# Optimization experiments

Measured on AMD Instinct MI355X. Metric: run time of the kernel, lower is better.

## Reference

```python
import jax, jax.numpy as jnp
import numpy as np

EMBED_DIM = 768
N_HEADS = 12
HEAD_DIM = EMBED_DIM // N_HEADS
B, S = 8, 1024


def setup_inputs() -> dict:
    key = jax.random.key(0)
    ks = jax.random.split(key, 7)
    sc = 1.0 / np.sqrt(HEAD_DIM)
    return {
        "sequences": jax.random.normal(ks[0], (B, S, EMBED_DIM), dtype=jnp.float32),
        # per-head Linear weights stored [H, in, out] (torch Linear is x @ W.T + b;
        # with random init the layout convention is equivalent math)
        "Wq": jax.random.normal(ks[1], (N_HEADS, HEAD_DIM, HEAD_DIM), dtype=jnp.float32) * sc,
        "bq": jax.random.normal(ks[2], (N_HEADS, HEAD_DIM), dtype=jnp.float32) * 0.01,
        "Wk": jax.random.normal(ks[3], (N_HEADS, HEAD_DIM, HEAD_DIM), dtype=jnp.float32) * sc,
        "bk": jax.random.normal(ks[4], (N_HEADS, HEAD_DIM), dtype=jnp.float32) * 0.01,
        "Wv": jax.random.normal(ks[5], (N_HEADS, HEAD_DIM, HEAD_DIM), dtype=jnp.float32) * sc,
        "bv": jax.random.normal(ks[6], (N_HEADS, HEAD_DIM), dtype=jnp.float32) * 0.01,
    }


def reference(sequences, Wq, bq, Wk, bk, Wv, bv):
    b, s, d = sequences.shape
    h, hd = Wq.shape[0], Wq.shape[1]
    x = sequences.reshape(b, s, h, hd)              # split embed dim into heads
    q = jnp.einsum("bshd,hde->bshe", x, Wq) + bq    # per-head linear (block-diag GEMM)
    k = jnp.einsum("bshd,hde->bshe", x, Wk) + bk
    v = jnp.einsum("bshd,hde->bshe", x, Wv) + bv
    # NOTE: original module applies NO 1/sqrt(head_dim) scaling
    logits = jnp.einsum("bshe,bthe->bhst", q, k)    # [B,H,S,S]
    attn = jax.nn.softmax(logits, axis=-1)
    out = jnp.einsum("bhst,bthe->bshe", attn, v)    # [B,S,H,hd]
    return out.reshape(b, s, d)
```

## Files before the change

### kernel.cpp

```cpp
#include <hip/hip_runtime.h>
#include <stdint.h>

#define EMBED 768
#define NH 12
#define HD 64
#define Bsz 8
#define Ssz 1024
#define LOG2E 1.44269504088896f

typedef __attribute__((ext_vector_type(4))) float f32x4;
typedef __attribute__((ext_vector_type(16))) float f32x16;
typedef __attribute__((ext_vector_type(8))) _Float16 f16x8;
typedef __attribute__((ext_vector_type(4))) _Float16 f16x4;
typedef __attribute__((ext_vector_type(2))) _Float16 f16x2;
typedef __attribute__((ext_vector_type(2))) __fp16 h16x2;
typedef __attribute__((ext_vector_type(4))) unsigned int u32x4;
typedef __attribute__((ext_vector_type(2))) unsigned int u32x2;

__launch_bounds__(256)
__global__ void qkv_proj(const float* __restrict__ x,
                         const float* __restrict__ Wq, const float* __restrict__ bq,
                         const float* __restrict__ Wk, const float* __restrict__ bk,
                         const float* __restrict__ Wv, const float* __restrict__ bv,
                         _Float16* __restrict__ Qb, _Float16* __restrict__ Kb,
                         _Float16* __restrict__ Vt)
{
    __shared__ _Float16 XT[128 * 72];
    __shared__ _Float16 Wt[3 * 64 * 72];
    __shared__ float Bs[192];

    const int bt = blockIdx.x;
    const int st = bt & 7;
    const int h  = (bt >> 3) % NH;
    const int b  = bt / (8 * NH);
    const int sbase = st * 128;
    const int tid = threadIdx.x;
    const int lane = tid & 63, w = tid >> 6;
    const int l15 = lane & 15, quad = lane >> 4;

    for (int i = 0; i < 8; ++i) {
        int idx = tid + 256 * i;
        int row = idx >> 4;
        int c4  = (idx & 15) * 4;
        const float4 g = *(const float4*)&x[(size_t)(b * Ssz + sbase + row) * EMBED + h * HD + c4];
        f16x4 v; v[0] = (_Float16)g.x; v[1] = (_Float16)g.y; v[2] = (_Float16)g.z; v[3] = (_Float16)g.w;
        *(f16x4*)&XT[row * 72 + c4] = v;
    }
    {
        const float* Ws0[3] = {Wq, Wk, Wv};
        const float* bs0[3] = {bq, bk, bv};
#pragma unroll
        for (int m = 0; m < 3; ++m) {
            const float* W = Ws0[m] + (size_t)h * HD * HD;
            for (int i = 0; i < 4; ++i) {
                int idx = tid + 256 * i;
                int d = idx >> 4, e4 = (idx & 15) * 4;
                float4 g = *(const float4*)&W[d * 64 + e4];
                Wt[m * 4608 + (e4 + 0) * 72 + d] = (_Float16)g.x;
                Wt[m * 4608 + (e4 + 1) * 72 + d] = (_Float16)g.y;
                Wt[m * 4608 + (e4 + 2) * 72 + d] = (_Float16)g.z;
                Wt[m * 4608 + (e4 + 3) * 72 + d] = (_Float16)g.w;
            }
        }
        if (tid < 192) Bs[tid] = bs0[tid >> 6][h * HD + (tid & 63)];
    }
    __syncthreads();

    f16x8 bx[2][2];
    const int nbg0 = w * 2;
#pragma unroll
    for (int nb = 0; nb < 2; ++nb)
#pragma unroll
        for (int kh = 0; kh < 2; ++kh)
            bx[nb][kh] = *(const f16x8*)&XT[((nbg0 + nb) * 16 + l15) * 72 + kh * 32 + quad * 8];
    __syncthreads();

    const size_t qkbase = (size_t)(b * NH + h) * Ssz + sbase;
    const f32x4 zero = {0.f, 0.f, 0.f, 0.f};

#pragma unroll
    for (int m = 0; m < 3; ++m) {
        f32x4 acc[2][4];
#pragma unroll
        for (int nb = 0; nb < 2; ++nb)
#pragma unroll
            for (int eb = 0; eb < 4; ++eb) acc[nb][eb] = zero;
#pragma unroll
        for (int eb = 0; eb < 4; ++eb)
#pragma unroll
            for (int kh = 0; kh < 2; ++kh) {
                f16x8 aw = *(const f16x8*)&Wt[m * 4608 + (eb * 16 + l15) * 72 + kh * 32 + quad * 8];
#pragma unroll
                for (int nb = 0; nb < 2; ++nb)
                    acc[nb][eb] = __builtin_amdgcn_mfma_f32_16x16x32_f16(aw, bx[nb][kh], acc[nb][eb], 0, 0, 0);
            }

        if (m < 2) {
            const float sc = (m == 0) ? LOG2E : 1.0f;
#pragma unroll
            for (int nb = 0; nb < 2; ++nb)
#pragma unroll
                for (int eb = 0; eb < 4; ++eb) {
                    f32x4 bb = *(const f32x4*)&Bs[m * 64 + eb * 16 + quad * 4];
                    f16x4 v;
#pragma unroll
                    for (int r = 0; r < 4; ++r) v[r] = (_Float16)((acc[nb][eb][r] + bb[r]) * sc);
                    *(f16x4*)&XT[((nbg0 + nb) * 16 + l15) * 72 + eb * 16 + quad * 4] = v;
                }
            __syncthreads();
            _Float16* outp = (m == 0) ? Qb : Kb;
            for (int i = 0; i < 4; ++i) {
                int idx = tid + 256 * i;
                int s = idx >> 3, e8 = (idx & 7) * 8;
                *(f16x8*)&outp[(qkbase + s) * HD + e8] = *(const f16x8*)&XT[s * 72 + e8];
            }
            __syncthreads();
        } else {
            _Float16* Vs = XT;
#pragma unroll
            for (int nb = 0; nb < 2; ++nb)
#pragma unroll
                for (int eb = 0; eb < 4; ++eb) {
                    f32x4 bb = *(const f32x4*)&Bs[128 + eb * 16 + quad * 4];
#pragma unroll
                    for (int r = 0; r < 4; ++r)
                        Vs[(eb * 16 + quad * 4 + r) * 136 + (nbg0 + nb) * 16 + l15] =
                            (_Float16)(acc[nb][eb][r] + bb[r]);
                }
            __syncthreads();
            for (int i = 0; i < 4; ++i) {
                int idx = tid + 256 * i;
                int e = idx >> 4, s8 = (idx & 15) * 8;
                *(f16x8*)&Vt[((size_t)(b * NH + h) * 64 + e) * Ssz + sbase + s8] =
                    *(const f16x8*)&Vs[e * 136 + s8];
            }
        }
    }
}

#define KVB 8192
__launch_bounds__(256, 2)
__global__ void attn(const _Float16* __restrict__ Qb, const _Float16* __restrict__ Kb,
                     const _Float16* __restrict__ Vt, float* __restrict__ out)
{
    __shared__ _Float16 KV[3 * KVB];

    const int bt = blockIdx.x;
    const int hh = bt % 96;
    const int qt = bt / 96;
    const int h  = hh % NH;
    const int b  = hh / NH;

    const int tid  = threadIdx.x;
    const int lane = tid & 63, w = tid >> 6;
    const int l31  = lane & 31;
    const int hf   = lane >> 5;

    const size_t bh = (size_t)(b * NH + h);
    const _Float16* Qg = Qb + bh * Ssz * HD;
    const _Float16* Kg = Kb + bh * Ssz * HD;
    const _Float16* Vg = Vt + bh * (size_t)HD * Ssz;

    const int qrow = qt * 128 + w * 32 + l31;
    f16x8 aq[4];
#pragma unroll
    for (int kk = 0; kk < 4; ++kk)
        aq[kk] = *(const f16x8*)&Qg[(size_t)qrow * HD + kk * 16 + hf * 8];

    const int ca = tid, cb = tid + 256;
    const int ra = ca >> 3, ga = (ca & 7) ^ (ra & 7);
    const int rb = cb >> 3, gb = (cb & 7) ^ (rb & 7);
    const _Float16* Ka  = Kg + ra * HD + ga * 8;
    const _Float16* Kb2 = Kg + rb * HD + gb * 8;
    const _Float16* Va  = Vg + (size_t)ra * Ssz + ga * 8;
    const _Float16* Vb  = Vg + (size_t)rb * Ssz + gb * 8;

#define STAGE(buf, kt_) do {                                                            \
    __builtin_amdgcn_global_load_lds(                                                   \
        (const __attribute__((address_space(1))) void*)(Ka + (kt_) * 64 * HD),          \
        (__attribute__((address_space(3))) void*)&KV[(buf) * KVB + ca * 8], 16, 0, 0);  \
    __builtin_amdgcn_global_load_lds(                                                   \
        (const __attribute__((address_space(1))) void*)(Kb2 + (kt_) * 64 * HD),         \
        (__attribute__((address_space(3))) void*)&KV[(buf) * KVB + cb * 8], 16, 0, 0);  \
    __builtin_amdgcn_global_load_lds(                                                   \
        (const __attribute__((address_space(1))) void*)(Va + (kt_) * 64),               \
        (__attribute__((address_space(3))) void*)&KV[(buf) * KVB + 4096 + ca * 8], 16, 0, 0); \
    __builtin_amdgcn_global_load_lds(                                                   \
        (const __attribute__((address_space(1))) void*)(Vb + (kt_) * 64),               \
        (__attribute__((address_space(3))) void*)&KV[(buf) * KVB + 4096 + cb * 8], 16, 0, 0); \
} while (0)

    const int rsw = l31 * 64;
    const int sx  = (l31 & 7) << 3;
    const int ch  = hf * 8;

    STAGE(0, 0);
    STAGE(1, 1);

    f32x16 o0, o1, zero16;
#pragma unroll
    for (int i = 0; i < 16; ++i) { o0[i] = 0.f; o1[i] = 0.f; zero16[i] = 0.f; }
    float m_run = -INFINITY;
    float la = 0.f, lb = 0.f, lc = 0.f, ld = 0.f;
    h16x2 ones2; ones2[0] = (__fp16)1.0f; ones2[1] = (__fp16)1.0f;

    __asm__ __volatile__("s_waitcnt vmcnt(4)" ::: "memory");
    __syncthreads();

#pragma unroll
    for (int kt = 0; kt < 16; ++kt) {
        const int bc = kt % 3;
        const int bs = (kt + 2) % 3;

        if (kt < 14) STAGE(bs, kt + 2);

        const _Float16* Ksb = &KV[bc * KVB];
        const _Float16* Vsb = &KV[bc * KVB + 4096];

        f32x16 st0, st1;
        __builtin_amdgcn_s_setprio(1);
        {
            const int col0 = ch ^ sx;
            f16x8 ak0 = *(const f16x8*)&Ksb[rsw + col0];
            f16x8 ak1 = *(const f16x8*)&Ksb[2048 + rsw + col0];
            st0 = __builtin_amdgcn_mfma_f32_32x32x16_f16(ak0, aq[0], zero16, 0, 0, 0);
            st1 = __builtin_amdgcn_mfma_f32_32x32x16_f16(ak1, aq[0], zero16, 0, 0, 0);
        }
#pragma unroll
        for (int kk = 1; kk < 4; ++kk) {
            const int col = (kk * 16 + ch) ^ sx;
            f16x8 ak0 = *(const f16x8*)&Ksb[rsw + col];
            f16x8 ak1 = *(const f16x8*)&Ksb[2048 + rsw + col];
            st0 = __builtin_amdgcn_mfma_f32_32x32x16_f16(ak0, aq[kk], st0, 0, 0, 0);
            st1 = __builtin_amdgcn_mfma_f32_32x32x16_f16(ak1, aq[kk], st1, 0, 0, 0);
        }
        __builtin_amdgcn_s_setprio(0);

        float m8[8];
#pragma unroll
        for (int i = 0; i < 8; ++i)
            m8[i] = fmaxf(fmaxf(st0[i], st0[i + 8]), fmaxf(st1[i], st1[i + 8]));
        float m4a = fmaxf(m8[0], m8[4]), m4b = fmaxf(m8[1], m8[5]);
        float m4c = fmaxf(m8[2], m8[6]), m4d = fmaxf(m8[3], m8[7]);
        float mt = fmaxf(fmaxf(m4a, m4b), fmaxf(m4c, m4d));
        mt = fmaxf(mt, __shfl_xor(mt, 32, 64));

        if (__any(mt > m_run + 8.f)) {
            float mn = fmaxf(m_run, mt);
            float al = __builtin_amdgcn_exp2f(m_run - mn);
            m_run = mn;
            la *= al; lb *= al; lc *= al; ld *= al;
#pragma unroll
            for (int i = 0; i < 16; ++i) { o0[i] *= al; o1[i] *= al; }
        }

#pragma unroll
        for (int i = 0; i < 16; ++i) st0[i] = __builtin_amdgcn_exp2f(st0[i] - m_run);
#pragma unroll
        for (int i = 0; i < 16; ++i) st1[i] = __builtin_amdgcn_exp2f(st1[i] - m_run);

        __builtin_amdgcn_s_setprio(1);
#pragma unroll
        for (int kk = 0; kk < 4; ++kk) {
            const f32x16& pp = (kk < 2) ? st0 : st1;
            const int c = 8 * (kk & 1);
            h16x2 x0h = __builtin_amdgcn_cvt_pkrtz(pp[c+0], pp[c+1]);
            h16x2 x1h = __builtin_amdgcn_cvt_pkrtz(pp[c+2], pp[c+3]);
            h16x2 y0h = __builtin_amdgcn_cvt_pkrtz(pp[c+4], pp[c+5]);
            h16x2 y1h = __builtin_amdgcn_cvt_pkrtz(pp[c+6], pp[c+7]);
            la = __builtin_amdgcn_fdot2(x0h, ones2, la, false);
            lb = __builtin_amdgcn_fdot2(x1h, ones2, lb, false);
            lc = __builtin_amdgcn_fdot2(y0h, ones2, lc, false);
            ld = __builtin_amdgcn_fdot2(y1h, ones2, ld, false);
            unsigned X0 = __builtin_bit_cast(unsigned, x0h);
            unsigned X1 = __builtin_bit_cast(unsigned, x1h);
            unsigned Y0 = __builtin_bit_cast(unsigned, y0h);
            unsigned Y1 = __builtin_bit_cast(unsigned, y1h);
            u32x2 r02 = __builtin_amdgcn_permlane32_swap(X0, Y0, 0, 0);
            u32x2 r13 = __builtin_amdgcn_permlane32_swap(X1, Y1, 0, 0);
            u32x4 du = {r02[0], r13[0], r02[1], r13[1]};
            f16x8 bp = __builtin_bit_cast(f16x8, du);
            const int col = (kk * 16 + ch) ^ sx;
            f16x8 av0 = *(const f16x8*)&Vsb[rsw + col];
            f16x8 av1 = *(const f16x8*)&Vsb[2048 + rsw + col];
            o0 = __builtin_amdgcn_mfma_f32_32x32x16_f16(av0, bp, o0, 0, 0, 0);
            o1 = __builtin_amdgcn_mfma_f32_32x32x16_f16(av1, bp, o1, 0, 0, 0);
        }
        __builtin_amdgcn_s_setprio(0);

        if (kt < 14) {
            __asm__ __volatile__("s_waitcnt vmcnt(4)" ::: "memory");
            __syncthreads();
        } else if (kt < 15) {
            __asm__ __volatile__("s_waitcnt vmcnt(0)" ::: "memory");
            __syncthreads();
        }
    }

    float l_run = (la + lb) + (lc + ld);
    l_run += __shfl_xor(l_run, 32, 64);
    const float inv = 1.f / l_run;
    float* op = &out[((size_t)b * Ssz + qrow) * EMBED + h * HD];
#pragma unroll
    for (int r1 = 0; r1 < 4; ++r1) {
        f32x4 v0, v1;
#pragma unroll
        for (int r0 = 0; r0 < 4; ++r0) {
            v0[r0] = o0[4 * r1 + r0] * inv;
            v1[r0] = o1[4 * r1 + r0] * inv;
        }
        *(f32x4*)&op[r1 * 8 + hf * 4]      = v0;
        *(f32x4*)&op[32 + r1 * 8 + hf * 4] = v1;
    }
#undef STAGE
}

extern "C" void kernel_launch(void* const* d_in, const int* in_sizes, int n_in,
                              void* d_out, int out_size, void* d_ws, size_t ws_size,
                              hipStream_t stream) {
    const float* x  = (const float*)d_in[0];
    const float* Wq = (const float*)d_in[1];
    const float* bq = (const float*)d_in[2];
    const float* Wk = (const float*)d_in[3];
    const float* bk = (const float*)d_in[4];
    const float* Wv = (const float*)d_in[5];
    const float* bv = (const float*)d_in[6];

    _Float16* Qb = (_Float16*)d_ws;
    _Float16* Kb = Qb + (size_t)Bsz * NH * Ssz * HD;
    _Float16* Vt = Kb + (size_t)Bsz * NH * Ssz * HD;

    qkv_proj<<<dim3(Bsz * NH * 8), dim3(256), 0, stream>>>(x, Wq, bq, Wk, bk, Wv, bv, Qb, Kb, Vt);
    attn<<<dim3(Bsz * NH * 8), dim3(256), 0, stream>>>(Qb, Kb, Vt, (float*)d_out);
}
```

Baseline: 130.1 us.

## Fuse Q projection into attention kernel and switch KV staging to double buffer

The Q projection moves out of the projection kernel and into the attention kernel. Each attention block converts its own x tile and Wq to fp16 in LDS and computes Q with MFMA, so Q is no longer written to and re-read from the workspace. The K/V staging pipeline shrinks from triple to double buffering with a full vmcnt(0) wait every iteration, the kt loop is no longer unrolled, and the min-blocks-per-SM launch bound is dropped. This saves a Q round trip through global memory, but it adds per-block projection work in front of attention and exposes more load latency because less prefetch runs ahead.

After: 147.2 us. 13.1% more time.

```diff
diff --git a/kernel.cpp b/kernel.cpp
--- a/kernel.cpp
+++ b/kernel.cpp
@@ -17,17 +17,16 @@
 typedef __attribute__((ext_vector_type(4))) unsigned int u32x4;
 typedef __attribute__((ext_vector_type(2))) unsigned int u32x2;
 
+
 __launch_bounds__(256)
-__global__ void qkv_proj(const float* __restrict__ x,
-                         const float* __restrict__ Wq, const float* __restrict__ bq,
-                         const float* __restrict__ Wk, const float* __restrict__ bk,
-                         const float* __restrict__ Wv, const float* __restrict__ bv,
-                         _Float16* __restrict__ Qb, _Float16* __restrict__ Kb,
-                         _Float16* __restrict__ Vt)
+__global__ void kv_proj(const float* __restrict__ x,
+                        const float* __restrict__ Wk, const float* __restrict__ bk,
+                        const float* __restrict__ Wv, const float* __restrict__ bv,
+                        _Float16* __restrict__ Kb, _Float16* __restrict__ Vt)
 {
     __shared__ _Float16 XT[128 * 72];
-    __shared__ _Float16 Wt[3 * 64 * 72];
-    __shared__ float Bs[192];
+    __shared__ _Float16 Wt[2 * 64 * 72];
+    __shared__ float Bs[128];
 
     const int bt = blockIdx.x;
     const int st = bt & 7;
@@ -46,24 +45,21 @@
         f16x4 v; v[0] = (_Float16)g.x; v[1] = (_Float16)g.y; v[2] = (_Float16)g.z; v[3] = (_Float16)g.w;
         *(f16x4*)&XT[row * 72 + c4] = v;
     }
-    {
-        const float* Ws0[3] = {Wq, Wk, Wv};
-        const float* bs0[3] = {bq, bk, bv};
-#pragma unroll
-        for (int m = 0; m < 3; ++m) {
-            const float* W = Ws0[m] + (size_t)h * HD * HD;
-            for (int i = 0; i < 4; ++i) {
-                int idx = tid + 256 * i;
-                int d = idx >> 4, e4 = (idx & 15) * 4;
-                float4 g = *(const float4*)&W[d * 64 + e4];
-                Wt[m * 4608 + (e4 + 0) * 72 + d] = (_Float16)g.x;
-                Wt[m * 4608 + (e4 + 1) * 72 + d] = (_Float16)g.y;
-                Wt[m * 4608 + (e4 + 2) * 72 + d] = (_Float16)g.z;
-                Wt[m * 4608 + (e4 + 3) * 72 + d] = (_Float16)g.w;
-            }
-        }
-        if (tid < 192) Bs[tid] = bs0[tid >> 6][h * HD + (tid & 63)];
-    }
+#pragma unroll
+    for (int m = 0; m < 2; ++m) {
+        const float* W = ((m == 0) ? Wk : Wv) + (size_t)h * HD * HD;
+        for (int i = 0; i < 4; ++i) {
+            int idx = tid + 256 * i;
+            int d = idx >> 4, e4 = (idx & 15) * 4;
+            float4 g = *(const float4*)&W[d * 64 + e4];
+            Wt[m * 4608 + (e4 + 0) * 72 + d] = (_Float16)g.x;
+            Wt[m * 4608 + (e4 + 1) * 72 + d] = (_Float16)g.y;
+            Wt[m * 4608 + (e4 + 2) * 72 + d] = (_Float16)g.z;
+            Wt[m * 4608 + (e4 + 3) * 72 + d] = (_Float16)g.w;
+        }
+    }
+    if (tid < 64)       Bs[tid] = bk[h * HD + tid];
+    else if (tid < 128) Bs[tid] = bv[h * HD + (tid - 64)];
     __syncthreads();
 
     f16x8 bx[2][2];
@@ -75,11 +71,11 @@
             bx[nb][kh] = *(const f16x8*)&XT[((nbg0 + nb) * 16 + l15) * 72 + kh * 32 + quad * 8];
     __syncthreads();
 
-    const size_t qkbase = (size_t)(b * NH + h) * Ssz + sbase;
+    const size_t kbase = (size_t)(b * NH + h) * Ssz + sbase;
     const f32x4 zero = {0.f, 0.f, 0.f, 0.f};
 
 #pragma unroll
-    for (int m = 0; m < 3; ++m) {
+    for (int m = 0; m < 2; ++m) {
         f32x4 acc[2][4];
 #pragma unroll
         for (int nb = 0; nb < 2; ++nb)
@@ -95,24 +91,22 @@
                     acc[nb][eb] = __builtin_amdgcn_mfma_f32_16x16x32_f16(aw, bx[nb][kh], acc[nb][eb], 0, 0, 0);
             }
 
-        if (m < 2) {
-            const float sc = (m == 0) ? LOG2E : 1.0f;
+        if (m == 0) {
 #pragma unroll
             for (int nb = 0; nb < 2; ++nb)
 #pragma unroll
                 for (int eb = 0; eb < 4; ++eb) {
-                    f32x4 bb = *(const f32x4*)&Bs[m * 64 + eb * 16 + quad * 4];
+                    f32x4 bb = *(const f32x4*)&Bs[eb * 16 + quad * 4];
                     f16x4 v;
 #pragma unroll
-                    for (int r = 0; r < 4; ++r) v[r] = (_Float16)((acc[nb][eb][r] + bb[r]) * sc);
+                    for (int r = 0; r < 4; ++r) v[r] = (_Float16)(acc[nb][eb][r] + bb[r]);
                     *(f16x4*)&XT[((nbg0 + nb) * 16 + l15) * 72 + eb * 16 + quad * 4] = v;
                 }
             __syncthreads();
-            _Float16* outp = (m == 0) ? Qb : Kb;
             for (int i = 0; i < 4; ++i) {
                 int idx = tid + 256 * i;
                 int s = idx >> 3, e8 = (idx & 7) * 8;
-                *(f16x8*)&outp[(qkbase + s) * HD + e8] = *(const f16x8*)&XT[s * 72 + e8];
+                *(f16x8*)&Kb[(kbase + s) * HD + e8] = *(const f16x8*)&XT[s * 72 + e8];
             }
             __syncthreads();
         } else {
@@ -121,7 +115,7 @@
             for (int nb = 0; nb < 2; ++nb)
 #pragma unroll
                 for (int eb = 0; eb < 4; ++eb) {
-                    f32x4 bb = *(const f32x4*)&Bs[128 + eb * 16 + quad * 4];
+                    f32x4 bb = *(const f32x4*)&Bs[64 + eb * 16 + quad * 4];
 #pragma unroll
                     for (int r = 0; r < 4; ++r)
                         Vs[(eb * 16 + quad * 4 + r) * 136 + (nbg0 + nb) * 16 + l15] =
@@ -139,11 +133,14 @@
 }
 
 #define KVB 8192
-__launch_bounds__(256, 2)
-__global__ void attn(const _Float16* __restrict__ Qb, const _Float16* __restrict__ Kb,
-                     const _Float16* __restrict__ Vt, float* __restrict__ out)
+__launch_bounds__(256)
+__global__ void attn(const float* __restrict__ x,
+                     const float* __restrict__ Wq, const float* __restrict__ bq,
+                     const _Float16* __restrict__ Kb, const _Float16* __restrict__ Vt,
+                     float* __restrict__ out)
 {
-    __shared__ _Float16 KV[3 * KVB];
+    __shared__ _Float16 KV[2 * KVB];
+    __shared__ float Bsq[64];
 
     const int bt = blockIdx.x;
     const int hh = bt % 96;
@@ -155,17 +152,80 @@
     const int lane = tid & 63, w = tid >> 6;
     const int l31  = lane & 31;
     const int hf   = lane >> 5;
+    const int l15  = lane & 15, quad = lane >> 4;
 
     const size_t bh = (size_t)(b * NH + h);
-    const _Float16* Qg = Qb + bh * Ssz * HD;
     const _Float16* Kg = Kb + bh * Ssz * HD;
     const _Float16* Vg = Vt + bh * (size_t)HD * Ssz;
 
     const int qrow = qt * 128 + w * 32 + l31;
     f16x8 aq[4];
-#pragma unroll
-    for (int kk = 0; kk < 4; ++kk)
-        aq[kk] = *(const f16x8*)&Qg[(size_t)qrow * HD + kk * 16 + hf * 8];
+
+    {
+        _Float16* XT  = KV;
+        _Float16* WqT = KV + 9216;
+
+        for (int i = 0; i < 8; ++i) {
+            int idx = tid + 256 * i;
+            int row = idx >> 4;
+            int c4  = (idx & 15) * 4;
+            const float4 g = *(const float4*)&x[(size_t)(b * Ssz + qt * 128 + row) * EMBED + h * HD + c4];
+            f16x4 v; v[0] = (_Float16)g.x; v[1] = (_Float16)g.y; v[2] = (_Float16)g.z; v[3] = (_Float16)g.w;
+            *(f16x4*)&XT[row * 72 + c4] = v;
+        }
+        const float* W = Wq + (size_t)h * HD * HD;
+        for (int i = 0; i < 4; ++i) {
+            int idx = tid + 256 * i;
+            int d = idx >> 4, e4 = (idx & 15) * 4;
+            float4 g = *(const float4*)&W[d * 64 + e4];
+            WqT[(e4 + 0) * 72 + d] = (_Float16)g.x;
+            WqT[(e4 + 1) * 72 + d] = (_Float16)g.y;
+            WqT[(e4 + 2) * 72 + d] = (_Float16)g.z;
+            WqT[(e4 + 3) * 72 + d] = (_Float16)g.w;
+        }
+        if (tid < 64) Bsq[tid] = bq[h * HD + tid];
+        __syncthreads();
+
+        f16x8 bx[2][2];
+        const int nbg0 = w * 2;
+#pragma unroll
+        for (int nb = 0; nb < 2; ++nb)
+#pragma unroll
+            for (int kh = 0; kh < 2; ++kh)
+                bx[nb][kh] = *(const f16x8*)&XT[((nbg0 + nb) * 16 + l15) * 72 + kh * 32 + quad * 8];
+        __syncthreads();
+
+        f32x4 acc[2][4];
+        const f32x4 zero = {0.f, 0.f, 0.f, 0.f};
+#pragma unroll
+        for (int nb = 0; nb < 2; ++nb)
+#pragma unroll
+            for (int eb = 0; eb < 4; ++eb) acc[nb][eb] = zero;
+#pragma unroll
+        for (int eb = 0; eb < 4; ++eb)
+#pragma unroll
+            for (int kh = 0; kh < 2; ++kh) {
+                f16x8 aw = *(const f16x8*)&WqT[(eb * 16 + l15) * 72 + kh * 32 + quad * 8];
+#pragma unroll
+                for (int nb = 0; nb < 2; ++nb)
+                    acc[nb][eb] = __builtin_amdgcn_mfma_f32_16x16x32_f16(aw, bx[nb][kh], acc[nb][eb], 0, 0, 0);
+            }
+#pragma unroll
+        for (int nb = 0; nb < 2; ++nb)
+#pragma unroll
+            for (int eb = 0; eb < 4; ++eb) {
+                f32x4 bb = *(const f32x4*)&Bsq[eb * 16 + quad * 4];
+                f16x4 v;
+#pragma unroll
+                for (int r = 0; r < 4; ++r) v[r] = (_Float16)((acc[nb][eb][r] + bb[r]) * LOG2E);
+                *(f16x4*)&XT[((nbg0 + nb) * 16 + l15) * 72 + eb * 16 + quad * 4] = v;
+            }
+        __syncthreads();
+#pragma unroll
+        for (int kk = 0; kk < 4; ++kk)
+            aq[kk] = *(const f16x8*)&XT[(w * 32 + l31) * 72 + kk * 16 + hf * 8];
+        __syncthreads();
+    }
 
     const int ca = tid, cb = tid + 256;
     const int ra = ca >> 3, ga = (ca & 7) ^ (ra & 7);
@@ -195,7 +255,6 @@
     const int ch  = hf * 8;
 
     STAGE(0, 0);
-    STAGE(1, 1);
 
     f32x16 o0, o1, zero16;
 #pragma unroll
@@ -204,18 +263,15 @@
     float la = 0.f, lb = 0.f, lc = 0.f, ld = 0.f;
     h16x2 ones2; ones2[0] = (__fp16)1.0f; ones2[1] = (__fp16)1.0f;
 
-    __asm__ __volatile__("s_waitcnt vmcnt(4)" ::: "memory");
+    __asm__ __volatile__("s_waitcnt vmcnt(0)" ::: "memory");
     __syncthreads();
 
-#pragma unroll
     for (int kt = 0; kt < 16; ++kt) {
-        const int bc = kt % 3;
-        const int bs = (kt + 2) % 3;
-
-        if (kt < 14) STAGE(bs, kt + 2);
-
-        const _Float16* Ksb = &KV[bc * KVB];
-        const _Float16* Vsb = &KV[bc * KVB + 4096];
+        const int cur = kt & 1;
+        if (kt < 15) STAGE(cur ^ 1, kt + 1);
+
+        const _Float16* Ksb = &KV[cur * KVB];
+        const _Float16* Vsb = &KV[cur * KVB + 4096];
 
         f32x16 st0, st1;
         __builtin_amdgcn_s_setprio(1);
@@ -288,13 +344,8 @@
         }
         __builtin_amdgcn_s_setprio(0);
 
-        if (kt < 14) {
-            __asm__ __volatile__("s_waitcnt vmcnt(4)" ::: "memory");
-            __syncthreads();
-        } else if (kt < 15) {
-            __asm__ __volatile__("s_waitcnt vmcnt(0)" ::: "memory");
-            __syncthreads();
-        }
+        __asm__ __volatile__("s_waitcnt vmcnt(0)" ::: "memory");
+        __syncthreads();
     }
 
     float l_run = (la + lb) + (lc + ld);
@@ -326,10 +377,9 @@
     const float* Wv = (const float*)d_in[5];
     const float* bv = (const float*)d_in[6];
 
-    _Float16* Qb = (_Float16*)d_ws;
-    _Float16* Kb = Qb + (size_t)Bsz * NH * Ssz * HD;
+    _Float16* Kb = (_Float16*)d_ws;
     _Float16* Vt = Kb + (size_t)Bsz * NH * Ssz * HD;
 
-    qkv_proj<<<dim3(Bsz * NH * 8), dim3(256), 0, stream>>>(x, Wq, bq, Wk, bk, Wv, bv, Qb, Kb, Vt);
-    attn<<<dim3(Bsz * NH * 8), dim3(256), 0, stream>>>(Qb, Kb, Vt, (float*)d_out);
+    kv_proj<<<dim3(Bsz * NH * 8), dim3(256), 0, stream>>>(x, Wk, bk, Wv, bv, Kb, Vt);
+    attn<<<dim3(Bsz * NH * 8), dim3(256), 0, stream>>>(x, Wq, bq, Kb, Vt, (float*)d_out);
 }
```
